# Kernel optimization log

Measured on AMD Instinct MI355X. Metric: run time of the kernel, lower is better.

## Reference

```python
import jax, jax.numpy as jnp
import numpy as np

B, S, D = 4, 4096, 2048
R_SSM = 6                      # ar_ssm_max_rank hardcoded in block
R_FFN = max(D // 96, 4)        # UltraLowRankFFN rank = 21
EPS = 1e-6


def rmsnorm(x, w):
    rms = jnp.sqrt(jnp.mean(x * x, axis=-1, keepdims=True) + EPS)
    return w * (x / rms)


def setup_inputs() -> dict:
    key = jax.random.key(0)
    ks = jax.random.split(key, 8)
    x = jax.random.normal(ks[0], (B, S, D), dtype=jnp.float32)
    norm1_w = jnp.ones((D,), dtype=jnp.float32)
    norm2_w = jnp.ones((D,), dtype=jnp.float32)
    # low-rank semiseparable AR-SSM params: in-proj U, decays lam, out-proj V
    U = jax.random.normal(ks[1], (D, R_SSM), dtype=jnp.float32) / np.sqrt(D)
    lam = jax.random.normal(ks[2], (R_SSM,), dtype=jnp.float32)
    V = jax.random.normal(ks[3], (R_SSM, D), dtype=jnp.float32) / np.sqrt(R_SSM)
    # ultra low-rank FFN
    W1 = jax.random.normal(ks[4], (D, R_FFN), dtype=jnp.float32) / np.sqrt(D)
    W2 = jax.random.normal(ks[5], (R_FFN, D), dtype=jnp.float32) / np.sqrt(R_FFN)
    return {"x": x, "norm1_w": norm1_w, "U": U, "lam": lam, "V": V,
            "norm2_w": norm2_w, "W1": W1, "W2": W2}


def reference(x, norm1_w, U, lam, V, norm2_w, W1, W2):
    # --- sublayer 1: RMSNorm -> low-rank semiseparable AR-SSM scan -> residual ---
    xn = rmsnorm(x, norm1_w)                     # [B,S,D]
    u = jnp.einsum('bsd,dr->bsr', xn, U)         # [B,S,r] low-rank input proj
    a = jax.nn.sigmoid(lam)                      # [r] stable decays in (0,1)

    def step(h, u_t):
        h = a * h + u_t                          # h: [B,r]
        return h, h

    h0 = jnp.zeros((B, R_SSM), dtype=x.dtype)
    _, hs = jax.lax.scan(step, h0, jnp.swapaxes(u, 0, 1))  # hs: [S,B,r]
    y = jnp.einsum('sbr,rd->bsd', hs, V)         # out proj back to d_model
    x = x + y

    # --- sublayer 2: RMSNorm -> ultra low-rank FFN (d->r->d, GELU) -> residual ---
    xn2 = rmsnorm(x, norm2_w)
    ffn = jnp.einsum('bsr,rd->bsd', jax.nn.gelu(jnp.einsum('bsd,dr->bsr', xn2, W1)), W2)
    return x + ffn
```

## Files before the change

### kernel.cpp

```cpp
#include <hip/hip_runtime.h>
#include <math.h>

namespace {
constexpr int S_ = 4096, D_ = 2048;
constexpr int RS_ = 6, RF_ = 21;
constexpr float EPS_ = 1e-6f;

#define DPP_ADD_(v, ctrl) \
  v += __int_as_float(__builtin_amdgcn_update_dpp(0, __float_as_int(v), ctrl, 0xF, 0xF, true))

__device__ __forceinline__ float wave_sum(float v) {
  DPP_ADD_(v, 0x111);
  DPP_ADD_(v, 0x112);
  DPP_ADD_(v, 0x114);
  DPP_ADD_(v, 0x118);
  DPP_ADD_(v, 0x142);
  DPP_ADD_(v, 0x143);
  return __int_as_float(__builtin_amdgcn_readlane(__float_as_int(v), 63));
}

__device__ __forceinline__ float rdlane(float v, int l) {
  return __int_as_float(__builtin_amdgcn_readlane(__float_as_int(v), l));
}

__device__ __forceinline__ float sel_lane(float old, float val, int tgt, int lane) {
  return (lane == tgt) ? val : old;
}

__device__ __forceinline__ float gelu_f(float x) {
  float i2 = 1.5957691216057308f * fmaf(0.044715f * x * x, x, x);
  return x * __builtin_amdgcn_rcpf(1.f + __expf(-i2));
}

__device__ __forceinline__ float dot4(float4 a, float4 b) {
  return fmaf(a.x, b.x, fmaf(a.y, b.y, fmaf(a.z, b.z, a.w * b.w)));
}

__device__ __forceinline__ float4 fma4(float s, float4 a, float4 c) {
  return make_float4(fmaf(s, a.x, c.x), fmaf(s, a.y, c.y), fmaf(s, a.z, c.z),
                     fmaf(s, a.w, c.w));
}

__device__ __forceinline__ void ld4(float4 (&q)[4], const float* p) {
  q[0] = *(const float4*)(p);
  q[1] = *(const float4*)(p + 256);
  q[2] = *(const float4*)(p + 512);
  q[3] = *(const float4*)(p + 768);
}
}

extern "C" __global__ void k_prep(const float* __restrict__ W1, const float* __restrict__ U,
                                  const float* __restrict__ n1w, const float* __restrict__ n2w,
                                  float* __restrict__ w1t, float* __restrict__ ut) {
  int t = blockIdx.x * 256 + threadIdx.x;
  if (t < D_ * RF_) {
    int d = t / RF_, j = t - d * RF_;
    w1t[j * D_ + d] = W1[t] * n2w[d];
  }
  int t2 = t - D_ * RF_;
  if (t2 >= 0 && t2 < D_ * RS_) {
    int d = t2 / RS_, r = t2 - d * RS_;
    ut[r * D_ + d] = U[t2] * n1w[d];
  }
}

extern "C" __global__ __launch_bounds__(256, 6) void k_rms1(
    const float* __restrict__ x, const float* __restrict__ ut,
    float* __restrict__ u_t) {
  int tid = threadIdx.x, lane = tid & 63, wid = tid >> 6;
  int row0 = blockIdx.x * 8 + wid * 2;
  int b = row0 >> 12;
  int sb = row0 & (S_ - 1);
  int d0 = lane * 4;
  const float* xr = x + (size_t)row0 * D_ + d0;
  const float* up = ut + d0;

  float s2a = 0.f, s2b = 0.f;
  float pa0 = 0.f, pa1 = 0.f, pa2 = 0.f, pa3 = 0.f, pa4 = 0.f, pa5 = 0.f;
  float pb0 = 0.f, pb1 = 0.f, pb2 = 0.f, pb3 = 0.f, pb4 = 0.f, pb5 = 0.f;
#pragma unroll
  for (int k = 0; k < 8; ++k) {
    float4 xa = *(const float4*)(xr + k * 256);
    float4 xb = *(const float4*)(xr + D_ + k * 256);
    s2a += dot4(xa, xa);
    s2b += dot4(xb, xb);
    float4 u0 = *(const float4*)(up + 0 * D_ + k * 256);
    pa0 += dot4(xa, u0); pb0 += dot4(xb, u0);
    float4 u1 = *(const float4*)(up + 1 * D_ + k * 256);
    pa1 += dot4(xa, u1); pb1 += dot4(xb, u1);
    float4 u2 = *(const float4*)(up + 2 * D_ + k * 256);
    pa2 += dot4(xa, u2); pb2 += dot4(xb, u2);
    float4 u3 = *(const float4*)(up + 3 * D_ + k * 256);
    pa3 += dot4(xa, u3); pb3 += dot4(xb, u3);
    float4 u4 = *(const float4*)(up + 4 * D_ + k * 256);
    pa4 += dot4(xa, u4); pb4 += dot4(xb, u4);
    float4 u5 = *(const float4*)(up + 5 * D_ + k * 256);
    pa5 += dot4(xa, u5); pb5 += dot4(xb, u5);
  }
  float ra = rsqrtf(wave_sum(s2a) * (1.0f / D_) + EPS_);
  float rb = rsqrtf(wave_sum(s2b) * (1.0f / D_) + EPS_);
  float va0 = wave_sum(pa0) * ra, vb0 = wave_sum(pb0) * rb;
  float va1 = wave_sum(pa1) * ra, vb1 = wave_sum(pb1) * rb;
  float va2 = wave_sum(pa2) * ra, vb2 = wave_sum(pb2) * rb;
  float va3 = wave_sum(pa3) * ra, vb3 = wave_sum(pb3) * rb;
  float va4 = wave_sum(pa4) * ra, vb4 = wave_sum(pb4) * rb;
  float va5 = wave_sum(pa5) * ra, vb5 = wave_sum(pb5) * rb;

  float uv = 0.f;
  uv = sel_lane(uv, va0, 0, lane);  uv = sel_lane(uv, vb0, 1, lane);
  uv = sel_lane(uv, va1, 2, lane);  uv = sel_lane(uv, vb1, 3, lane);
  uv = sel_lane(uv, va2, 4, lane);  uv = sel_lane(uv, vb2, 5, lane);
  uv = sel_lane(uv, va3, 6, lane);  uv = sel_lane(uv, vb3, 7, lane);
  uv = sel_lane(uv, va4, 8, lane);  uv = sel_lane(uv, vb4, 9, lane);
  uv = sel_lane(uv, va5, 10, lane); uv = sel_lane(uv, vb5, 11, lane);
  if (lane < 2 * RS_) {
    int r = lane >> 1, w = lane & 1;
    u_t[((size_t)b * RS_ + r) * S_ + sb + w] = uv;
  }
}

extern "C" __global__ __launch_bounds__(64) void k_scan(
    const float* __restrict__ lam, const float* __restrict__ u_t,
    float* __restrict__ hs_t) {
  int br = blockIdx.x;
  int r = br % RS_;
  int lane = threadIdx.x;
  float a = 1.f / (1.f + __expf(-lam[r]));
  float a64 = a;
#pragma unroll
  for (int i = 0; i < 6; ++i) a64 *= a64;

  const float* ub = u_t + (size_t)br * S_ + lane * 64;
  float vloc = 0.f;
#pragma unroll
  for (int i = 0; i < 16; ++i) {
    float4 uu = *(const float4*)(ub + i * 4);
    vloc = fmaf(a, vloc, uu.x);
    vloc = fmaf(a, vloc, uu.y);
    vloc = fmaf(a, vloc, uu.z);
    vloc = fmaf(a, vloc, uu.w);
  }
  float m = a64, v = vloc;
#pragma unroll
  for (int off = 1; off < 64; off <<= 1) {
    float mu = __shfl_up(m, off);
    float vu = __shfl_up(v, off);
    if (lane >= off) {
      v = fmaf(m, vu, v);
      m *= mu;
    }
  }
  float carry = __shfl_up(v, 1);
  if (lane == 0) carry = 0.f;

  float h = carry;
  float* hb = hs_t + (size_t)br * S_ + lane * 64;
#pragma unroll
  for (int i = 0; i < 16; ++i) {
    float4 uu = *(const float4*)(ub + i * 4);
    float4 o;
    h = fmaf(a, h, uu.x); o.x = h;
    h = fmaf(a, h, uu.y); o.y = h;
    h = fmaf(a, h, uu.z); o.z = h;
    h = fmaf(a, h, uu.w); o.w = h;
    *(float4*)(hb + i * 4) = o;
  }
}

extern "C" __global__ __launch_bounds__(256, 2) void k_main(
    const float* __restrict__ x, const float* __restrict__ V,
    const float* __restrict__ w1t, const float* __restrict__ W2,
    const float* __restrict__ hs_t, float* __restrict__ out) {
  int tid = threadIdx.x, lane = tid & 63, wid = tid >> 6;
  int row0 = blockIdx.x * 16 + wid * 4;
  int b = row0 >> 12;
  int s0 = row0 & (S_ - 1);
  int d0 = lane * 4;

  float hv = 0.f;
  if (lane < 4 * RS_) {
    int w = lane / RS_, r = lane - w * RS_;
    hv = hs_t[((size_t)b * RS_ + r) * S_ + s0 + w];
  }

  float4 xv[4][8];
  const float* xr = x + (size_t)row0 * D_ + d0;
#pragma unroll
  for (int w = 0; w < 4; ++w)
#pragma unroll
    for (int k = 0; k < 8; ++k)
      xv[w][k] = *(const float4*)(xr + w * D_ + k * 256);

  float4 qA[4], qB[4];

  const float* Vp = V + d0;
  ld4(qA, Vp);
#pragma unroll 2
  for (int r = 0; r < RS_; ++r) {
    ld4(qB, Vp + r * D_ + 1024);
    float h0 = rdlane(hv, 0 * RS_ + r), h1 = rdlane(hv, 1 * RS_ + r);
    float h2 = rdlane(hv, 2 * RS_ + r), h3 = rdlane(hv, 3 * RS_ + r);
#pragma unroll
    for (int k = 0; k < 4; ++k) {
      xv[0][k] = fma4(h0, qA[k], xv[0][k]);
      xv[1][k] = fma4(h1, qA[k], xv[1][k]);
      xv[2][k] = fma4(h2, qA[k], xv[2][k]);
      xv[3][k] = fma4(h3, qA[k], xv[3][k]);
    }
    if (r + 1 < RS_) ld4(qA, Vp + (r + 1) * D_);
#pragma unroll
    for (int k = 0; k < 4; ++k) {
      xv[0][4 + k] = fma4(h0, qB[k], xv[0][4 + k]);
      xv[1][4 + k] = fma4(h1, qB[k], xv[1][4 + k]);
      xv[2][4 + k] = fma4(h2, qB[k], xv[2][4 + k]);
      xv[3][4 + k] = fma4(h3, qB[k], xv[3][4 + k]);
    }
  }

  float s20 = 0.f, s21 = 0.f, s22 = 0.f, s23 = 0.f;
#pragma unroll
  for (int k = 0; k < 8; ++k) {
    s20 += dot4(xv[0][k], xv[0][k]);
    s21 += dot4(xv[1][k], xv[1][k]);
    s22 += dot4(xv[2][k], xv[2][k]);
    s23 += dot4(xv[3][k], xv[3][k]);
  }
  float rinv0 = rsqrtf(wave_sum(s20) * (1.0f / D_) + EPS_);
  float rinv1 = rsqrtf(wave_sum(s21) * (1.0f / D_) + EPS_);
  float rinv2 = rsqrtf(wave_sum(s22) * (1.0f / D_) + EPS_);
  float rinv3 = rsqrtf(wave_sum(s23) * (1.0f / D_) + EPS_);

  float g0 = 0.f, g1 = 0.f, g2 = 0.f, g3 = 0.f;
  const float* Wp = w1t + d0;
  ld4(qA, Wp);
#pragma unroll 3
  for (int j = 0; j < RF_; ++j) {
    ld4(qB, Wp + j * D_ + 1024);
    float p0 = 0.f, p1 = 0.f, p2 = 0.f, p3 = 0.f;
#pragma unroll
    for (int k = 0; k < 4; ++k) {
      p0 += dot4(xv[0][k], qA[k]);
      p1 += dot4(xv[1][k], qA[k]);
      p2 += dot4(xv[2][k], qA[k]);
      p3 += dot4(xv[3][k], qA[k]);
    }
    if (j + 1 < RF_) ld4(qA, Wp + (j + 1) * D_);
#pragma unroll
    for (int k = 0; k < 4; ++k) {
      p0 += dot4(xv[0][4 + k], qB[k]);
      p1 += dot4(xv[1][4 + k], qB[k]);
      p2 += dot4(xv[2][4 + k], qB[k]);
      p3 += dot4(xv[3][4 + k], qB[k]);
    }
    float t0 = wave_sum(p0) * rinv0;
    float t1 = wave_sum(p1) * rinv1;
    float t2 = wave_sum(p2) * rinv2;
    float t3 = wave_sum(p3) * rinv3;
    g0 = sel_lane(g0, t0, j, lane);
    g1 = sel_lane(g1, t1, j, lane);
    g2 = sel_lane(g2, t2, j, lane);
    g3 = sel_lane(g3, t3, j, lane);
  }
  g0 = gelu_f(g0); g1 = gelu_f(g1); g2 = gelu_f(g2); g3 = gelu_f(g3);

  const float* W2p = W2 + d0;
  ld4(qA, W2p);
#pragma unroll 3
  for (int j = 0; j < RF_; ++j) {
    ld4(qB, W2p + j * D_ + 1024);
    float f0 = rdlane(g0, j), f1 = rdlane(g1, j);
    float f2 = rdlane(g2, j), f3 = rdlane(g3, j);
#pragma unroll
    for (int k = 0; k < 4; ++k) {
      xv[0][k] = fma4(f0, qA[k], xv[0][k]);
      xv[1][k] = fma4(f1, qA[k], xv[1][k]);
      xv[2][k] = fma4(f2, qA[k], xv[2][k]);
      xv[3][k] = fma4(f3, qA[k], xv[3][k]);
    }
    if (j + 1 < RF_) ld4(qA, W2p + (j + 1) * D_);
#pragma unroll
    for (int k = 0; k < 4; ++k) {
      xv[0][4 + k] = fma4(f0, qB[k], xv[0][4 + k]);
      xv[1][4 + k] = fma4(f1, qB[k], xv[1][4 + k]);
      xv[2][4 + k] = fma4(f2, qB[k], xv[2][4 + k]);
      xv[3][4 + k] = fma4(f3, qB[k], xv[3][4 + k]);
    }
  }

  float* orow = out + (size_t)row0 * D_ + d0;
#pragma unroll
  for (int w = 0; w < 4; ++w)
#pragma unroll
    for (int k = 0; k < 8; ++k)
      *(float4*)(orow + w * D_ + k * 256) = xv[w][k];
}

extern "C" void kernel_launch(void* const* d_in, const int* in_sizes, int n_in,
                              void* d_out, int out_size, void* d_ws, size_t ws_size,
                              hipStream_t stream) {
  const float* x   = (const float*)d_in[0];
  const float* n1w = (const float*)d_in[1];
  const float* U   = (const float*)d_in[2];
  const float* lam = (const float*)d_in[3];
  const float* V   = (const float*)d_in[4];
  const float* n2w = (const float*)d_in[5];
  const float* W1  = (const float*)d_in[6];
  const float* W2  = (const float*)d_in[7];
  float* out = (float*)d_out;
  float* ws  = (float*)d_ws;

  float* u_t  = ws;
  float* hs_t = ws + 98304;
  float* w1t  = ws + 196608;
  float* ut   = ws + 239616;

  k_prep<<<216, 256, 0, stream>>>(W1, U, n1w, n2w, w1t, ut);
  k_rms1<<<2048, 256, 0, stream>>>(x, ut, u_t);
  k_scan<<<24, 64, 0, stream>>>(lam, u_t, hs_t);
  k_main<<<1024, 256, 0, stream>>>(x, V, w1t, W2, hs_t, out);
}
```

Before: 338.8 us.

## Stage weight rows in shared memory per block and raise occupancy target

Weight rows for V, W1 and W2 are now copied cooperatively into a 32 KB shared buffer, four rows at a time, and read from LDS. Before, each of the four waves loaded the same rows straight from global memory, and the loads were software-pipelined. Launch bounds go from 2 to 3 blocks per CU, which pushes the register budget down while each wave still holds 128 floats of x in registers. The aim is fewer redundant global or L2 weight reads. The cost is many __syncthreads barriers with no overlap between copy and compute, and a risk of register spills.

```diff
diff --git a/kernel.cpp b/kernel.cpp
--- a/kernel.cpp
+++ b/kernel.cpp
@@ -39,13 +39,6 @@
 __device__ __forceinline__ float4 fma4(float s, float4 a, float4 c) {
   return make_float4(fmaf(s, a.x, c.x), fmaf(s, a.y, c.y), fmaf(s, a.z, c.z),
                      fmaf(s, a.w, c.w));
-}
-
-__device__ __forceinline__ void ld4(float4 (&q)[4], const float* p) {
-  q[0] = *(const float4*)(p);
-  q[1] = *(const float4*)(p + 256);
-  q[2] = *(const float4*)(p + 512);
-  q[3] = *(const float4*)(p + 768);
 }
 }
 
@@ -167,10 +160,12 @@
   }
 }
 
-extern "C" __global__ __launch_bounds__(256, 2) void k_main(
+extern "C" __global__ __launch_bounds__(256, 3) void k_main(
     const float* __restrict__ x, const float* __restrict__ V,
     const float* __restrict__ w1t, const float* __restrict__ W2,
     const float* __restrict__ hs_t, float* __restrict__ out) {
+  __shared__ float wbuf[4 * D_];
+
   int tid = threadIdx.x, lane = tid & 63, wid = tid >> 6;
   int row0 = blockIdx.x * 16 + wid * 4;
   int b = row0 >> 12;
@@ -191,29 +186,28 @@
     for (int k = 0; k < 8; ++k)
       xv[w][k] = *(const float4*)(xr + w * D_ + k * 256);
 
-  float4 qA[4], qB[4];
-
-  const float* Vp = V + d0;
-  ld4(qA, Vp);
-#pragma unroll 2
-  for (int r = 0; r < RS_; ++r) {
-    ld4(qB, Vp + r * D_ + 1024);
-    float h0 = rdlane(hv, 0 * RS_ + r), h1 = rdlane(hv, 1 * RS_ + r);
-    float h2 = rdlane(hv, 2 * RS_ + r), h3 = rdlane(hv, 3 * RS_ + r);
-#pragma unroll
-    for (int k = 0; k < 4; ++k) {
-      xv[0][k] = fma4(h0, qA[k], xv[0][k]);
-      xv[1][k] = fma4(h1, qA[k], xv[1][k]);
-      xv[2][k] = fma4(h2, qA[k], xv[2][k]);
-      xv[3][k] = fma4(h3, qA[k], xv[3][k]);
-    }
-    if (r + 1 < RS_) ld4(qA, Vp + (r + 1) * D_);
-#pragma unroll
-    for (int k = 0; k < 4; ++k) {
-      xv[0][4 + k] = fma4(h0, qB[k], xv[0][4 + k]);
-      xv[1][4 + k] = fma4(h1, qB[k], xv[1][4 + k]);
-      xv[2][4 + k] = fma4(h2, qB[k], xv[2][4 + k]);
-      xv[3][4 + k] = fma4(h3, qB[k], xv[3][4 + k]);
+  for (int r0 = 0; r0 < RS_; r0 += 4) {
+    int cnt = (RS_ - r0 < 4) ? (RS_ - r0) : 4;
+    __syncthreads();
+    {
+      const float4* src = (const float4*)(V + r0 * D_);
+      float4* dst = (float4*)wbuf;
+      for (int i = tid; i < cnt * (D_ / 4); i += 256) dst[i] = src[i];
+    }
+    __syncthreads();
+    for (int rr = 0; rr < cnt; ++rr) {
+      int r = r0 + rr;
+      const float* wr = wbuf + rr * D_ + d0;
+      float h0 = rdlane(hv, 0 * RS_ + r), h1 = rdlane(hv, 1 * RS_ + r);
+      float h2 = rdlane(hv, 2 * RS_ + r), h3 = rdlane(hv, 3 * RS_ + r);
+#pragma unroll
+      for (int k = 0; k < 8; ++k) {
+        float4 q = *(const float4*)(wr + k * 256);
+        xv[0][k] = fma4(h0, q, xv[0][k]);
+        xv[1][k] = fma4(h1, q, xv[1][k]);
+        xv[2][k] = fma4(h2, q, xv[2][k]);
+        xv[3][k] = fma4(h3, q, xv[3][k]);
+      }
     }
   }
 
@@ -231,59 +225,61 @@
   float rinv3 = rsqrtf(wave_sum(s23) * (1.0f / D_) + EPS_);
 
   float g0 = 0.f, g1 = 0.f, g2 = 0.f, g3 = 0.f;
-  const float* Wp = w1t + d0;
-  ld4(qA, Wp);
-#pragma unroll 3
-  for (int j = 0; j < RF_; ++j) {
-    ld4(qB, Wp + j * D_ + 1024);
-    float p0 = 0.f, p1 = 0.f, p2 = 0.f, p3 = 0.f;
-#pragma unroll
-    for (int k = 0; k < 4; ++k) {
-      p0 += dot4(xv[0][k], qA[k]);
-      p1 += dot4(xv[1][k], qA[k]);
-      p2 += dot4(xv[2][k], qA[k]);
-      p3 += dot4(xv[3][k], qA[k]);
-    }
-    if (j + 1 < RF_) ld4(qA, Wp + (j + 1) * D_);
-#pragma unroll
-    for (int k = 0; k < 4; ++k) {
-      p0 += dot4(xv[0][4 + k], qB[k]);
-      p1 += dot4(xv[1][4 + k], qB[k]);
-      p2 += dot4(xv[2][4 + k], qB[k]);
-      p3 += dot4(xv[3][4 + k], qB[k]);
-    }
-    float t0 = wave_sum(p0) * rinv0;
-    float t1 = wave_sum(p1) * rinv1;
-    float t2 = wave_sum(p2) * rinv2;
-    float t3 = wave_sum(p3) * rinv3;
-    g0 = sel_lane(g0, t0, j, lane);
-    g1 = sel_lane(g1, t1, j, lane);
-    g2 = sel_lane(g2, t2, j, lane);
-    g3 = sel_lane(g3, t3, j, lane);
+  for (int j0 = 0; j0 < RF_; j0 += 4) {
+    int cnt = (RF_ - j0 < 4) ? (RF_ - j0) : 4;
+    __syncthreads();
+    {
+      const float4* src = (const float4*)(w1t + j0 * D_);
+      float4* dst = (float4*)wbuf;
+      for (int i = tid; i < cnt * (D_ / 4); i += 256) dst[i] = src[i];
+    }
+    __syncthreads();
+    for (int jj = 0; jj < cnt; ++jj) {
+      const float* wr = wbuf + jj * D_ + d0;
+      float p0 = 0.f, p1 = 0.f, p2 = 0.f, p3 = 0.f;
+#pragma unroll
+      for (int k = 0; k < 8; ++k) {
+        float4 q = *(const float4*)(wr + k * 256);
+        p0 += dot4(xv[0][k], q);
+        p1 += dot4(xv[1][k], q);
+        p2 += dot4(xv[2][k], q);
+        p3 += dot4(xv[3][k], q);
+      }
+      int j = j0 + jj;
+      float t0 = wave_sum(p0) * rinv0;
+      float t1 = wave_sum(p1) * rinv1;
+      float t2 = wave_sum(p2) * rinv2;
+      float t3 = wave_sum(p3) * rinv3;
+      g0 = sel_lane(g0, t0, j, lane);
+      g1 = sel_lane(g1, t1, j, lane);
+      g2 = sel_lane(g2, t2, j, lane);
+      g3 = sel_lane(g3, t3, j, lane);
+    }
   }
   g0 = gelu_f(g0); g1 = gelu_f(g1); g2 = gelu_f(g2); g3 = gelu_f(g3);
 
-  const float* W2p = W2 + d0;
-  ld4(qA, W2p);
-#pragma unroll 3
-  for (int j = 0; j < RF_; ++j) {
-    ld4(qB, W2p + j * D_ + 1024);
-    float f0 = rdlane(g0, j), f1 = rdlane(g1, j);
-    float f2 = rdlane(g2, j), f3 = rdlane(g3, j);
-#pragma unroll
-    for (int k = 0; k < 4; ++k) {
-      xv[0][k] = fma4(f0, qA[k], xv[0][k]);
-      xv[1][k] = fma4(f1, qA[k], xv[1][k]);
-      xv[2][k] = fma4(f2, qA[k], xv[2][k]);
-      xv[3][k] = fma4(f3, qA[k], xv[3][k]);
-    }
-    if (j + 1 < RF_) ld4(qA, W2p + (j + 1) * D_);
-#pragma unroll
-    for (int k = 0; k < 4; ++k) {
-      xv[0][4 + k] = fma4(f0, qB[k], xv[0][4 + k]);
-      xv[1][4 + k] = fma4(f1, qB[k], xv[1][4 + k]);
-      xv[2][4 + k] = fma4(f2, qB[k], xv[2][4 + k]);
-      xv[3][4 + k] = fma4(f3, qB[k], xv[3][4 + k]);
+  for (int j0 = 0; j0 < RF_; j0 += 4) {
+    int cnt = (RF_ - j0 < 4) ? (RF_ - j0) : 4;
+    __syncthreads();
+    {
+      const float4* src = (const float4*)(W2 + j0 * D_);
+      float4* dst = (float4*)wbuf;
+      for (int i = tid; i < cnt * (D_ / 4); i += 256) dst[i] = src[i];
+    }
+    __syncthreads();
+    for (int jj = 0; jj < cnt; ++jj) {
+      int j = j0 + jj;
+      const float* wr = wbuf + jj * D_ + d0;
+      float f0 = rdlane(g0, j), f1 = rdlane(g1, j);
+      float f2 = rdlane(g2, j), f3 = rdlane(g3, j);
+#pragma unroll
+      for (int k = 0; k < 8; ++k) {
+        float4 q = *(const float4*)(wr + k * 256);
+        xv[0][k] = fma4(f0, q, xv[0][k]);
+        xv[1][k] = fma4(f1, q, xv[1][k]);
+        xv[2][k] = fma4(f2, q, xv[2][k]);
+        xv[3][k] = fma4(f3, q, xv[3][k]);
+      }
     }
   }
 
```

Result: slower. 373.7 us (+10.3%).
